# Kernel optimization log

Measured on AMD Instinct MI355X. Metric: run time of the kernel, lower is better.

Reference implementation:

```python
import jax, jax.numpy as jnp
import numpy as np

B, LD, LE = 32, 256, 258          # batch, decoder len (split_num), encoder len (split_num+2)
ENC, DEC, HID = 512, 512, 512     # encoder_size, decoder_size(=GRU hidden), GRU hidden
MLP, NL = 256, 4                  # biaffine mlp size, num transition labels


def setup_inputs() -> dict:
    key = jax.random.key(0)
    ks = jax.random.split(key, 12)
    s = 0.05  # modest init scale for stability
    return {
        "e_outputs": jax.random.normal(ks[0], (B, LE, ENC), jnp.float32),
        "d_inputs": jax.random.normal(ks[1], (B, LD, HID), jnp.float32),
        "h0": jax.random.normal(ks[2], (B, HID), jnp.float32),
        "W_ih": jax.random.normal(ks[3], (3 * HID, HID), jnp.float32) * s,
        "W_hh": jax.random.normal(ks[4], (3 * HID, HID), jnp.float32) * s,
        "b_ih": jnp.zeros((3 * HID,), jnp.float32),
        "b_hh": jnp.zeros((3 * HID,), jnp.float32),
        "e_mlp_w": jax.random.normal(ks[5], (MLP, ENC), jnp.float32) * s,
        "e_mlp_b": jnp.zeros((MLP,), jnp.float32),
        "d_mlp_w": jax.random.normal(ks[6], (MLP, DEC), jnp.float32) * s,
        "d_mlp_b": jnp.zeros((MLP,), jnp.float32),
        "W_e": jax.random.normal(ks[7], (NL, MLP), jnp.float32) * s,
        "W_d": jax.random.normal(ks[8], (NL, MLP), jnp.float32) * s,
        "U": jax.random.normal(ks[9], (NL, MLP, MLP), jnp.float32) * s,
        "b_aff": jnp.zeros((NL, 1, 1), jnp.float32),
    }


def reference(e_outputs, d_inputs, h0, W_ih, W_hh, b_ih, b_hh,
              e_mlp_w, e_mlp_b, d_mlp_w, d_mlp_b, W_e, W_d, U, b_aff):
    def gru_step(h, x):
        gi = x @ W_ih.T + b_ih            # (B, 3H)
        gh = h @ W_hh.T + b_hh            # (B, 3H)
        i_r, i_z, i_n = jnp.split(gi, 3, axis=-1)
        h_r, h_z, h_n = jnp.split(gh, 3, axis=-1)
        r = jax.nn.sigmoid(i_r + h_r)
        z = jax.nn.sigmoid(i_z + h_z)
        n = jnp.tanh(i_n + r * h_n)
        h_new = (1.0 - z) * n + z * h
        return h_new, h_new

    xs = jnp.swapaxes(d_inputs, 0, 1)     # (LD, B, HID)
    _, hs = jax.lax.scan(gru_step, h0, xs)
    d_outputs = jnp.swapaxes(hs, 0, 1)    # (B, LD, HID)

    # --- biaffine pointer scoring (BiAffineAttention.forward) ---
    e_h = jax.nn.relu(e_outputs @ e_mlp_w.T + e_mlp_b)   # (B, LE, MLP)
    d_h = jax.nn.relu(d_outputs @ d_mlp_w.T + d_mlp_b)   # (B, LD, MLP)

    out_e = jnp.einsum('lh,beh->ble', W_e, e_h)[:, :, None, :]   # (B, NL, 1, LE)
    out_d = jnp.einsum('lh,bdh->bld', W_d, d_h)[:, :, :, None]   # (B, NL, LD, 1)
    out_u = jnp.einsum('bdh,lhk,bek->blde', d_h, U, e_h)         # (B, NL, LD, LE)

    out = out_e + out_d + out_u + b_aff                          # b_aff: (NL,1,1)
    return jnp.transpose(out, (0, 2, 3, 1))                      # (B, LD, LE, NL)
```

## Files before the change

### kernel.cpp

```cpp
#include <hip/hip_runtime.h>
#include <hip/hip_fp16.h>
#include <math.h>

#define NB   32
#define LD   256
#define LE   258
#define HID  512
#define H3   1536
#define MLP  256
#define NL   4
#define FLAG_STRIDE 32

typedef _Float16 h2 __attribute__((ext_vector_type(2)));

__global__ void k_init(uint32_t* __restrict__ flags){
  for (int i = threadIdx.x; i < NB*8*FLAG_STRIDE; i += 256) flags[i] = 0u;
}

__global__ __launch_bounds__(192,1)
void k_gru(const float* __restrict__ GI, const float* __restrict__ W_hh,
           const float* __restrict__ b_hh, const float* __restrict__ h0,
           float* __restrict__ dout, float* __restrict__ hbuf,
           uint32_t* __restrict__ flags){
  const int wg  = blockIdx.x;
  const int b   = wg >> 3, g = wg & 7;
  const int tid = threadIdx.x;
  const int sect = tid >> 6;
  const int u    = tid & 63;
  const int c    = sect*HID + g*64 + u;

  __shared__ __align__(16) float h_lds[HID];
  __shared__ float zs[64], gs[64], ns[64];

  h2 w[256];
  const float4* wr = (const float4*)(W_hh + (size_t)c*HID);
  #pragma unroll
  for (int i=0;i<128;i++){
    float4 v = wr[i];
    h2 p0; p0[0]=(_Float16)v.x; p0[1]=(_Float16)v.y;
    h2 p1; p1[0]=(_Float16)v.z; p1[1]=(_Float16)v.w;
    w[2*i] = p0; w[2*i+1] = p1;
  }
  const float bh = b_hh[c];
  float h_old = (tid < 64) ? h0[(size_t)b*HID + g*64 + u] : 0.f;
  const float* gi_base = GI + (size_t)b*LD*H3 + c;
  uint32_t* fb = flags + (size_t)b*8*FLAG_STRIDE;
  float* db = dout + (size_t)b*LD*HID + g*64;

  for (int i=tid;i<HID;i+=192) h_lds[i] = h0[(size_t)b*HID + i];
  __syncthreads();

  float gi = gi_base[0];
  for (int t=0;t<LD;t++){
    float a0=0.f, a1=0.f, a2=0.f, a3=0.f;
    const float4* hl = (const float4*)h_lds;
    #pragma unroll
    for (int kk=0;kk<128;kk++){
      float4 hv = hl[kk];
      h2 w0 = w[2*kk], w1 = w[2*kk+1];
      a0 = fmaf((float)w0[0], hv.x, a0);
      a1 = fmaf((float)w0[1], hv.y, a1);
      a2 = fmaf((float)w1[0], hv.z, a2);
      a3 = fmaf((float)w1[1], hv.w, a3);
    }
    float hh = (a0+a1) + (a2+a3) + bh;
    if (sect==1)      zs[u] = gi + hh;
    else if (sect==2){ gs[u] = gi; ns[u] = hh; }
    float pre_r = gi + hh;
    __syncthreads();
    float hnew = 0.f;
    if (tid < 64){
      float r = __builtin_amdgcn_rcpf(1.f + __expf(-pre_r));
      float z = __builtin_amdgcn_rcpf(1.f + __expf(-zs[u]));
      float x = gs[u] + r*ns[u];
      float e2 = __expf(2.f*x);
      float n = 1.f - 2.f*__builtin_amdgcn_rcpf(e2 + 1.f);
      hnew = (1.f-z)*n + z*h_old;
      h_old = hnew;
    }
    if (t < LD-1){
      float* hb = hbuf + (size_t)((t+1)&1)*(NB*HID) + (size_t)b*HID;
      if (tid < 64){
        __hip_atomic_store(hb + g*64 + u, hnew,
                           __ATOMIC_RELAXED, __HIP_MEMORY_SCOPE_AGENT);
        asm volatile("s_waitcnt vmcnt(0)" ::: "memory");
        if (tid == 0)
          __hip_atomic_store(fb + g*FLAG_STRIDE, (uint32_t)(t+1),
                             __ATOMIC_RELAXED, __HIP_MEMORY_SCOPE_AGENT);
        db[(size_t)t*HID + u] = hnew;
      }
      gi = gi_base[(size_t)(t+1)*H3];
      if (tid >= 64 && tid < 72){
        int s = tid - 64;
        int guard = 0;
        while (__hip_atomic_load(fb + s*FLAG_STRIDE, __ATOMIC_RELAXED,
                                 __HIP_MEMORY_SCOPE_AGENT) < (uint32_t)(t+1)
               && guard < (1<<20)){ __builtin_amdgcn_s_sleep(1); ++guard; }
      }
      __syncthreads();
      for (int i=tid;i<HID;i+=192)
        h_lds[i] = __hip_atomic_load(hb+i, __ATOMIC_RELAXED, __HIP_MEMORY_SCOPE_AGENT);
      __syncthreads();
    } else {
      if (tid < 64) db[(size_t)t*HID + u] = hnew;
    }
  }
}

template<int BIAS, int RELU>
__global__ __launch_bounds__(256)
void k_gemm_nt(const float* __restrict__ A, const float* __restrict__ Bm,
               const float* __restrict__ bias, float* __restrict__ C,
               int M, int N, int K){
  __shared__ float As[32][68];
  __shared__ float Bs[32][68];
  const int bm = blockIdx.y*64, bn = blockIdx.x*64;
  const int tid = threadIdx.x;
  const int tx = tid & 15, ty = tid >> 4;
  const int lr = tid >> 3;
  const int lk = (tid & 7) << 2;
  const float* A0 = A + (size_t)(bm+lr)*K + lk;
  const float* A1 = A + (size_t)(bm+lr+32)*K + lk;
  const float* B0 = Bm + (size_t)(bn+lr)*K + lk;
  const float* B1 = Bm + (size_t)(bn+lr+32)*K + lk;
  float acc[4][4] = {};
  for (int k0=0;k0<K;k0+=32){
    float4 a0 = *(const float4*)(A0 + k0);
    float4 a1 = *(const float4*)(A1 + k0);
    float4 b0 = *(const float4*)(B0 + k0);
    float4 b1 = *(const float4*)(B1 + k0);
    __syncthreads();
    As[lk+0][lr]=a0.x; As[lk+1][lr]=a0.y; As[lk+2][lr]=a0.z; As[lk+3][lr]=a0.w;
    As[lk+0][lr+32]=a1.x; As[lk+1][lr+32]=a1.y; As[lk+2][lr+32]=a1.z; As[lk+3][lr+32]=a1.w;
    Bs[lk+0][lr]=b0.x; Bs[lk+1][lr]=b0.y; Bs[lk+2][lr]=b0.z; Bs[lk+3][lr]=b0.w;
    Bs[lk+0][lr+32]=b1.x; Bs[lk+1][lr+32]=b1.y; Bs[lk+2][lr+32]=b1.z; Bs[lk+3][lr+32]=b1.w;
    __syncthreads();
    #pragma unroll
    for (int kk=0;kk<32;kk++){
      float4 av = *(const float4*)&As[kk][ty<<2];
      float4 bv = *(const float4*)&Bs[kk][tx<<2];
      float a4[4] = {av.x,av.y,av.z,av.w};
      float b4[4] = {bv.x,bv.y,bv.z,bv.w};
      #pragma unroll
      for (int i=0;i<4;i++)
        #pragma unroll
        for (int j=0;j<4;j++)
          acc[i][j] = fmaf(a4[i], b4[j], acc[i][j]);
    }
  }
  #pragma unroll
  for (int i=0;i<4;i++){
    int m = bm + (ty<<2) + i;
    #pragma unroll
    for (int j=0;j<4;j++){
      int n = bn + (tx<<2) + j;
      float v = acc[i][j];
      if (BIAS) v += bias[n];
      if (RELU) v = fmaxf(v, 0.f);
      C[(size_t)m*N + n] = v;
    }
  }
}

__global__ __launch_bounds__(256)
void k_gemm_nn_T(const float* __restrict__ A, const float* __restrict__ U,
                 float* __restrict__ T){
  __shared__ float As[32][68];
  __shared__ float Bs[32][68];
  const int l = blockIdx.z;
  const float* Bm = U + (size_t)l*MLP*MLP;
  float* C = T + (size_t)l*NB*LD*MLP;
  const int bm = blockIdx.y*64, bn = blockIdx.x*64;
  const int tid = threadIdx.x;
  const int tx = tid & 15, ty = tid >> 4;
  const int lr = tid >> 3;
  const int lk = (tid & 7) << 2;
  const int bk_r = tid >> 4;
  const int bn_c = (tid & 15) << 2;
  const float* A0 = A + (size_t)(bm+lr)*MLP + lk;
  const float* A1 = A + (size_t)(bm+lr+32)*MLP + lk;
  float acc[4][4] = {};
  for (int k0=0;k0<MLP;k0+=32){
    float4 a0 = *(const float4*)(A0 + k0);
    float4 a1 = *(const float4*)(A1 + k0);
    float4 u0 = *(const float4*)(Bm + (size_t)(k0+bk_r)*MLP + bn + bn_c);
    float4 u1 = *(const float4*)(Bm + (size_t)(k0+bk_r+16)*MLP + bn + bn_c);
    __syncthreads();
    As[lk+0][lr]=a0.x; As[lk+1][lr]=a0.y; As[lk+2][lr]=a0.z; As[lk+3][lr]=a0.w;
    As[lk+0][lr+32]=a1.x; As[lk+1][lr+32]=a1.y; As[lk+2][lr+32]=a1.z; As[lk+3][lr+32]=a1.w;
    *(float4*)&Bs[bk_r][bn_c]    = u0;
    *(float4*)&Bs[bk_r+16][bn_c] = u1;
    __syncthreads();
    #pragma unroll
    for (int kk=0;kk<32;kk++){
      float4 av = *(const float4*)&As[kk][ty<<2];
      float4 bv = *(const float4*)&Bs[kk][tx<<2];
      float a4[4] = {av.x,av.y,av.z,av.w};
      float b4[4] = {bv.x,bv.y,bv.z,bv.w};
      #pragma unroll
      for (int i=0;i<4;i++)
        #pragma unroll
        for (int j=0;j<4;j++)
          acc[i][j] = fmaf(a4[i], b4[j], acc[i][j]);
    }
  }
  #pragma unroll
  for (int i=0;i<4;i++){
    int m = bm + (ty<<2) + i;
    #pragma unroll
    for (int j=0;j<4;j++)
      C[(size_t)m*MLP + bn + (tx<<2) + j] = acc[i][j];
  }
}

__global__ void k_bilinear(const float* __restrict__ W, const float* __restrict__ Hm,
                           float* __restrict__ S, int Lrows){
  int idx = blockIdx.x*256 + threadIdx.x;
  if (idx >= NB*Lrows) return;
  int b = idx / Lrows, r = idx - b*Lrows;
  const float* row = Hm + (size_t)idx*MLP;
  float acc[NL] = {0.f,0.f,0.f,0.f};
  for (int h=0; h<MLP; h+=4){
    float4 x = *(const float4*)(row + h);
    #pragma unroll
    for (int l=0;l<NL;l++){
      float4 w = *(const float4*)(W + l*MLP + h);
      acc[l] += x.x*w.x + x.y*w.y + x.z*w.z + x.w*w.w;
    }
  }
  #pragma unroll
  for (int l=0;l<NL;l++) S[((size_t)b*NL + l)*Lrows + r] = acc[l];
}

__global__ __launch_bounds__(256)
void k_s2(const float* __restrict__ T, const float* __restrict__ eh,
          const float* __restrict__ sd, const float* __restrict__ se,
          const float* __restrict__ baff, float* __restrict__ out){
  __shared__ float As[32][68];
  __shared__ float Bs[32][68];
  const int b = blockIdx.z;
  const int d0 = blockIdx.y*64, e0 = blockIdx.x*64;
  const int tid = threadIdx.x;
  const int tx = tid & 15, ty = tid >> 4;
  const int lr = tid >> 3;
  const int lk = (tid & 7) << 2;
  const float* EH = eh + (size_t)b*LE*MLP;
  for (int l=0;l<NL;l++){
    const float* A = T + ((size_t)(l*NB + b))*LD*MLP;
    float acc[4][4] = {};
    for (int k0=0;k0<MLP;k0+=32){
      float4 a0 = *(const float4*)(A + (size_t)(d0+lr)*MLP + k0 + lk);
      float4 a1 = *(const float4*)(A + (size_t)(d0+lr+32)*MLP + k0 + lk);
      float4 z4 = make_float4(0.f,0.f,0.f,0.f);
      int er0 = e0+lr, er1 = e0+lr+32;
      float4 b0 = (er0<LE) ? *(const float4*)(EH + (size_t)er0*MLP + k0 + lk) : z4;
      float4 b1 = (er1<LE) ? *(const float4*)(EH + (size_t)er1*MLP + k0 + lk) : z4;
      __syncthreads();
      As[lk+0][lr]=a0.x; As[lk+1][lr]=a0.y; As[lk+2][lr]=a0.z; As[lk+3][lr]=a0.w;
      As[lk+0][lr+32]=a1.x; As[lk+1][lr+32]=a1.y; As[lk+2][lr+32]=a1.z; As[lk+3][lr+32]=a1.w;
      Bs[lk+0][lr]=b0.x; Bs[lk+1][lr]=b0.y; Bs[lk+2][lr]=b0.z; Bs[lk+3][lr]=b0.w;
      Bs[lk+0][lr+32]=b1.x; Bs[lk+1][lr+32]=b1.y; Bs[lk+2][lr+32]=b1.z; Bs[lk+3][lr+32]=b1.w;
      __syncthreads();
      #pragma unroll
      for (int kk=0;kk<32;kk++){
        float4 av = *(const float4*)&As[kk][ty<<2];
        float4 bv = *(const float4*)&Bs[kk][tx<<2];
        float a4[4] = {av.x,av.y,av.z,av.w};
        float b4[4] = {bv.x,bv.y,bv.z,bv.w};
        #pragma unroll
        for (int i=0;i<4;i++)
          #pragma unroll
          for (int j=0;j<4;j++)
            acc[i][j] = fmaf(a4[i], b4[j], acc[i][j]);
      }
    }
    float bl = baff[l];
    float sdl[4], sel[4];
    #pragma unroll
    for (int i=0;i<4;i++) sdl[i] = sd[((size_t)b*NL + l)*LD + d0 + (ty<<2) + i];
    #pragma unroll
    for (int j=0;j<4;j++){
      int e = e0 + (tx<<2) + j;
      sel[j] = (e<LE) ? se[((size_t)b*NL + l)*LE + e] : 0.f;
    }
    #pragma unroll
    for (int i=0;i<4;i++){
      int d = d0 + (ty<<2) + i;
      #pragma unroll
      for (int j=0;j<4;j++){
        int e = e0 + (tx<<2) + j;
        if (e < LE)
          out[(((size_t)b*LD + d)*LE + e)*NL + l] = acc[i][j] + sdl[i] + sel[j] + bl;
      }
    }
  }
}

extern "C" void kernel_launch(void* const* d_in, const int* in_sizes, int n_in,
                              void* d_out, int out_size, void* d_ws, size_t ws_size,
                              hipStream_t stream){
  const float* e_outputs = (const float*)d_in[0];
  const float* d_inputs  = (const float*)d_in[1];
  const float* h0        = (const float*)d_in[2];
  const float* W_ih      = (const float*)d_in[3];
  const float* W_hh      = (const float*)d_in[4];
  const float* b_ih      = (const float*)d_in[5];
  const float* b_hh      = (const float*)d_in[6];
  const float* e_mlp_w   = (const float*)d_in[7];
  const float* e_mlp_b   = (const float*)d_in[8];
  const float* d_mlp_w   = (const float*)d_in[9];
  const float* d_mlp_b   = (const float*)d_in[10];
  const float* W_e       = (const float*)d_in[11];
  const float* W_d       = (const float*)d_in[12];
  const float* U         = (const float*)d_in[13];
  const float* b_aff     = (const float*)d_in[14];
  float* out = (float*)d_out;
  float* ws  = (float*)d_ws;

  float* GI   = ws;
  float* T    = ws;
  float* hbuf = ws + 12582912;
  uint32_t* flags = (uint32_t*)(hbuf + 2*NB*HID);
  float* dout = ws   + 12582912 + 786432;
  float* eh   = dout + 4194304;
  float* dh   = eh   + 2113536;
  float* se   = dh   + 2097152;
  float* sd   = se   + 33024;

  k_init<<<dim3(1), 256, 0, stream>>>(flags);
  k_gemm_nt<1,0><<<dim3(H3/64, (NB*LD)/64), 256, 0, stream>>>(d_inputs, W_ih, b_ih, GI, NB*LD, H3, HID);
  k_gemm_nt<1,1><<<dim3(MLP/64, (NB*LE)/64), 256, 0, stream>>>(e_outputs, e_mlp_w, e_mlp_b, eh, NB*LE, MLP, HID);
  k_gru<<<dim3(NB*8), 192, 0, stream>>>(GI, W_hh, b_hh, h0, dout, hbuf, flags);
  k_gemm_nt<1,1><<<dim3(MLP/64, (NB*LD)/64), 256, 0, stream>>>(dout, d_mlp_w, d_mlp_b, dh, NB*LD, MLP, HID);
  k_gemm_nn_T<<<dim3(MLP/64, (NB*LD)/64, NL), 256, 0, stream>>>(dh, U, T);
  k_bilinear<<<dim3((NB*LE+255)/256), 256, 0, stream>>>(W_e, eh, se, LE);
  k_bilinear<<<dim3((NB*LD+255)/256), 256, 0, stream>>>(W_d, dh, sd, LD);
  k_s2<<<dim3(5, LD/64, NB), 256, 0, stream>>>(T, eh, sd, se, b_aff, out);
}
```

Measured before the change: 2.801 ms.

## Embed step tag in hidden-state low bits to drop separate flag handshake

Removes the per-group flag word and the store-wait-flag sequence in the GRU inter-workgroup exchange. Each hidden value now carries a 3-bit step tag in its low mantissa bits, and every thread polls its own slice of the exchange buffer until all tags match, writing directly into LDS. This saves a round of memory latency and one barrier per step. In exchange it drops three mantissa bits of the hidden state fed into the recurrence, and it relies on a tag that wraps every eight steps, made safe only by double buffering.

```diff
diff --git a/kernel.cpp b/kernel.cpp
--- a/kernel.cpp
+++ b/kernel.cpp
@@ -9,19 +9,18 @@
 #define H3   1536
 #define MLP  256
 #define NL   4
-#define FLAG_STRIDE 32
 
 typedef _Float16 h2 __attribute__((ext_vector_type(2)));
 
-__global__ void k_init(uint32_t* __restrict__ flags){
-  for (int i = threadIdx.x; i < NB*8*FLAG_STRIDE; i += 256) flags[i] = 0u;
+__global__ void k_init(uint32_t* __restrict__ hbuf){
+  int i = blockIdx.x*256 + threadIdx.x;
+  if (i < 2*NB*HID) hbuf[i] = 0u;
 }
 
 __global__ __launch_bounds__(192,1)
 void k_gru(const float* __restrict__ GI, const float* __restrict__ W_hh,
            const float* __restrict__ b_hh, const float* __restrict__ h0,
-           float* __restrict__ dout, float* __restrict__ hbuf,
-           uint32_t* __restrict__ flags){
+           float* __restrict__ dout, float* __restrict__ hbuf){
   const int wg  = blockIdx.x;
   const int b   = wg >> 3, g = wg & 7;
   const int tid = threadIdx.x;
@@ -44,8 +43,9 @@
   const float bh = b_hh[c];
   float h_old = (tid < 64) ? h0[(size_t)b*HID + g*64 + u] : 0.f;
   const float* gi_base = GI + (size_t)b*LD*H3 + c;
-  uint32_t* fb = flags + (size_t)b*8*FLAG_STRIDE;
   float* db = dout + (size_t)b*LD*HID + g*64;
+
+  const int w0 = tid, w1 = tid + 192, w2 = tid + 384;
 
   for (int i=tid;i<HID;i+=192) h_lds[i] = h0[(size_t)b*HID + i];
   __syncthreads();
@@ -57,52 +57,60 @@
     #pragma unroll
     for (int kk=0;kk<128;kk++){
       float4 hv = hl[kk];
-      h2 w0 = w[2*kk], w1 = w[2*kk+1];
-      a0 = fmaf((float)w0[0], hv.x, a0);
-      a1 = fmaf((float)w0[1], hv.y, a1);
-      a2 = fmaf((float)w1[0], hv.z, a2);
-      a3 = fmaf((float)w1[1], hv.w, a3);
+      h2 q0 = w[2*kk], q1 = w[2*kk+1];
+      a0 = fmaf((float)q0[0], hv.x, a0);
+      a1 = fmaf((float)q0[1], hv.y, a1);
+      a2 = fmaf((float)q1[0], hv.z, a2);
+      a3 = fmaf((float)q1[1], hv.w, a3);
     }
     float hh = (a0+a1) + (a2+a3) + bh;
     if (sect==1)      zs[u] = gi + hh;
     else if (sect==2){ gs[u] = gi; ns[u] = hh; }
     float pre_r = gi + hh;
     __syncthreads();
-    float hnew = 0.f;
-    if (tid < 64){
-      float r = __builtin_amdgcn_rcpf(1.f + __expf(-pre_r));
-      float z = __builtin_amdgcn_rcpf(1.f + __expf(-zs[u]));
-      float x = gs[u] + r*ns[u];
-      float e2 = __expf(2.f*x);
-      float n = 1.f - 2.f*__builtin_amdgcn_rcpf(e2 + 1.f);
-      hnew = (1.f-z)*n + z*h_old;
-      h_old = hnew;
-    }
+
     if (t < LD-1){
-      float* hb = hbuf + (size_t)((t+1)&1)*(NB*HID) + (size_t)b*HID;
+      float gnext = gi_base[(size_t)(t+1)*H3];
+      uint32_t* hb = (uint32_t*)(hbuf + (size_t)((t+1)&1)*(NB*HID) + (size_t)b*HID);
+      const uint32_t want = (uint32_t)(t+1) & 7u;
       if (tid < 64){
-        __hip_atomic_store(hb + g*64 + u, hnew,
+        float r = __builtin_amdgcn_rcpf(1.f + __expf(-pre_r));
+        float z = __builtin_amdgcn_rcpf(1.f + __expf(-zs[u]));
+        float x = gs[u] + r*ns[u];
+        float e2 = __expf(2.f*x);
+        float n = 1.f - 2.f*__builtin_amdgcn_rcpf(e2 + 1.f);
+        float hnew = (1.f-z)*n + z*h_old;
+        h_old = hnew;
+        uint32_t wb = (__builtin_bit_cast(uint32_t, hnew) & ~7u) | want;
+        __hip_atomic_store(hb + g*64 + u, wb,
                            __ATOMIC_RELAXED, __HIP_MEMORY_SCOPE_AGENT);
-        asm volatile("s_waitcnt vmcnt(0)" ::: "memory");
-        if (tid == 0)
-          __hip_atomic_store(fb + g*FLAG_STRIDE, (uint32_t)(t+1),
-                             __ATOMIC_RELAXED, __HIP_MEMORY_SCOPE_AGENT);
         db[(size_t)t*HID + u] = hnew;
       }
-      gi = gi_base[(size_t)(t+1)*H3];
-      if (tid >= 64 && tid < 72){
-        int s = tid - 64;
-        int guard = 0;
-        while (__hip_atomic_load(fb + s*FLAG_STRIDE, __ATOMIC_RELAXED,
-                                 __HIP_MEMORY_SCOPE_AGENT) < (uint32_t)(t+1)
-               && guard < (1<<20)){ __builtin_amdgcn_s_sleep(1); ++guard; }
+      uint32_t* hlu = (uint32_t*)h_lds;
+      bool ok = false; int guard = 0;
+      while (!ok && guard < (1<<17)){
+        uint32_t x0 = __hip_atomic_load(hb+w0, __ATOMIC_RELAXED, __HIP_MEMORY_SCOPE_AGENT);
+        uint32_t x1 = __hip_atomic_load(hb+w1, __ATOMIC_RELAXED, __HIP_MEMORY_SCOPE_AGENT);
+        uint32_t x2 = want;
+        if (w2 < HID)
+          x2 = __hip_atomic_load(hb+w2, __ATOMIC_RELAXED, __HIP_MEMORY_SCOPE_AGENT);
+        hlu[w0] = x0; hlu[w1] = x1;
+        if (w2 < HID) hlu[w2] = x2;
+        ok = ((x0&7u)==want) & ((x1&7u)==want) & ((x2&7u)==want);
+        if (!ok){ ++guard; __builtin_amdgcn_s_sleep(1); }
       }
       __syncthreads();
-      for (int i=tid;i<HID;i+=192)
-        h_lds[i] = __hip_atomic_load(hb+i, __ATOMIC_RELAXED, __HIP_MEMORY_SCOPE_AGENT);
-      __syncthreads();
+      gi = gnext;
     } else {
-      if (tid < 64) db[(size_t)t*HID + u] = hnew;
+      if (tid < 64){
+        float r = __builtin_amdgcn_rcpf(1.f + __expf(-pre_r));
+        float z = __builtin_amdgcn_rcpf(1.f + __expf(-zs[u]));
+        float x = gs[u] + r*ns[u];
+        float e2 = __expf(2.f*x);
+        float n = 1.f - 2.f*__builtin_amdgcn_rcpf(e2 + 1.f);
+        float hnew = (1.f-z)*n + z*h_old;
+        db[(size_t)t*HID + u] = hnew;
+      }
     }
   }
 }
@@ -320,17 +328,16 @@
   float* GI   = ws;
   float* T    = ws;
   float* hbuf = ws + 12582912;
-  uint32_t* flags = (uint32_t*)(hbuf + 2*NB*HID);
   float* dout = ws   + 12582912 + 786432;
   float* eh   = dout + 4194304;
   float* dh   = eh   + 2113536;
   float* se   = dh   + 2097152;
   float* sd   = se   + 33024;
 
-  k_init<<<dim3(1), 256, 0, stream>>>(flags);
+  k_init<<<dim3((2*NB*HID+255)/256), 256, 0, stream>>>((uint32_t*)hbuf);
   k_gemm_nt<1,0><<<dim3(H3/64, (NB*LD)/64), 256, 0, stream>>>(d_inputs, W_ih, b_ih, GI, NB*LD, H3, HID);
   k_gemm_nt<1,1><<<dim3(MLP/64, (NB*LE)/64), 256, 0, stream>>>(e_outputs, e_mlp_w, e_mlp_b, eh, NB*LE, MLP, HID);
-  k_gru<<<dim3(NB*8), 192, 0, stream>>>(GI, W_hh, b_hh, h0, dout, hbuf, flags);
+  k_gru<<<dim3(NB*8), 192, 0, stream>>>(GI, W_hh, b_hh, h0, dout, hbuf);
   k_gemm_nt<1,1><<<dim3(MLP/64, (NB*LD)/64), 256, 0, stream>>>(dout, d_mlp_w, d_mlp_b, dh, NB*LD, MLP, HID);
   k_gemm_nn_T<<<dim3(MLP/64, (NB*LD)/64, NL), 256, 0, stream>>>(dh, U, T);
   k_bilinear<<<dim3((NB*LE+255)/256), 256, 0, stream>>>(W_e, eh, se, LE);
```

Result: faster. 2.518 ms (-10.1%).
